# Performance work log

Measured on AMD Instinct MI355X. Metric: run time of the kernel, lower is better.

## Reference

```python
import math
import jax, jax.numpy as jnp
import numpy as np

NUM_HEADS = 8
HIDDEN = 512
HEAD_DIM = HIDDEN // NUM_HEADS
LEFT_CONTEXT = 128
RIGHT_CONTEXT = 0


def setup_inputs() -> dict:
    key = jax.random.key(0)
    k1, k2, k3 = jax.random.split(key, 3)
    queries = jax.random.normal(k1, (4, 64, 128, NUM_HEADS, HEAD_DIM), dtype=jnp.float32)
    keys = jax.random.normal(k2, (4, 64, 256, NUM_HEADS, HEAD_DIM), dtype=jnp.float32)
    # pos_proj weight, torch Linear layout [out_features, in_features]
    W_pos = jax.random.normal(k3, (NUM_HEADS * HEAD_DIM, HIDDEN), dtype=jnp.float32) * (1.0 / math.sqrt(HIDDEN))
    return {"queries": queries, "keys": keys, "W_pos": W_pos}


def reference(queries, keys, W_pos):
    batch, num_blocks, block_size, num_heads, head_dim = queries.shape
    context = keys.shape[2]
    left = max(0, LEFT_CONTEXT - 1)
    right = RIGHT_CONTEXT

    # q: [b, h, n, s, d]; k: [b, h, n, d, c]
    q = jnp.transpose(queries, (0, 3, 1, 2, 4))
    k = jnp.transpose(keys, (0, 3, 1, 4, 2))
    term_ac = jnp.matmul(q, k)  # [b, h, n, s, c]

    # sinusoidal relative-position embeddings for offsets left .. -right
    positions = jnp.arange(left, -right - 1, -1, dtype=jnp.float32)  # [P]
    num_timescales = HIDDEN // 2
    log_increment = math.log(10000.0) / max(num_timescales - 1, 1)
    inv_timescales = jnp.exp(jnp.arange(num_timescales, dtype=jnp.float32) * -log_increment)
    scaled_time = positions[:, None] * inv_timescales[None, :]  # [P, HIDDEN/2]
    sin_emb = jnp.concatenate([jnp.sin(scaled_time), jnp.cos(scaled_time)], axis=-1)  # [P, HIDDEN]

    # pos_proj (no bias): [P, H*D] -> [P, H, D]
    proj = (sin_emb @ W_pos.T).reshape(-1, num_heads, head_dim)
    pos_length = proj.shape[0]

    # term_bd: [b, h, n, s, P]
    term_bd = jnp.einsum('bhnsd,phd->bhnsp', q, proj)

    # Transformer-XL relative shift: pad, flatten, truncate, reshape
    pad = context + 1 - pos_length
    if pad > 0:
        term_bd = jnp.pad(term_bd, ((0, 0), (0, 0), (0, 0), (0, 0), (0, pad)))
    term_bd = term_bd.reshape(batch, num_heads, num_blocks, block_size * (context + 1))
    term_bd = term_bd[:, :, :, : block_size * context]
    term_bd = term_bd.reshape(batch, num_heads, num_blocks, block_size, context)

    return term_ac + term_bd
```

## Files before the change

kernel.cpp:

```cpp
#include <hip/hip_runtime.h>
#include <hip/hip_bf16.h>


typedef __bf16 bf16x8 __attribute__((ext_vector_type(8)));
typedef unsigned short u16x8 __attribute__((ext_vector_type(8)));
typedef unsigned int u32x4 __attribute__((ext_vector_type(4)));
typedef float f32x4 __attribute__((ext_vector_type(4)));

__device__ __forceinline__ unsigned short f2bf(float f) {
    unsigned u = __float_as_uint(f);
    u = (u + 0x7FFFu + ((u >> 16) & 1u)) >> 16;
    return (unsigned short)u;
}
__device__ __forceinline__ float bf2f(unsigned short s) {
    return __uint_as_float(((unsigned)s) << 16);
}
__device__ __forceinline__ unsigned pk2(float a, float b) {
    return (__float_as_uint(a) >> 16) | (__float_as_uint(b) & 0xFFFF0000u);
}

__global__ __launch_bounds__(256) void proj_kernel(const float* __restrict__ W,
                                                   unsigned short* __restrict__ projw) {
    __shared__ float se[512];
    int bid = blockIdx.x;
    int p  = bid >> 3;
    int jq = bid & 7;
    int t = threadIdx.x;
    const float LOGINC = (float)(9.210340371976184 / 255.0);
    float pos = (float)(127 - p);
    float inv = expf(-LOGINC * (float)t);
    float ang = pos * inv;
    se[t]       = sinf(ang);
    se[t + 256] = cosf(ang);
    __syncthreads();
    int j  = jq * 64 + (t >> 2);
    int tq = t & 3;
    const float4* wr = (const float4*)(W + (size_t)j * 512 + tq * 128);
    const float4* sr = (const float4*)(se + tq * 128);
    float a = 0.f;
#pragma unroll
    for (int i = 0; i < 32; ++i) {
        float4 wv = wr[i];
        float4 sv = sr[i];
        a += sv.x * wv.x + sv.y * wv.y + sv.z * wv.z + sv.w * wv.w;
    }
    a += __shfl_xor(a, 1);
    a += __shfl_xor(a, 2);
    if (tq == 0) projw[p * 512 + j] = f2bf(a);
}

__global__ __launch_bounds__(256, 4) void fused_kernel(const float* __restrict__ Q,
                                                       const float* __restrict__ Kg,
                                                       const unsigned short* __restrict__ projw,
                                                       float* __restrict__ out) {
    __shared__ unsigned short BDs[128 * 128];
    __shared__ unsigned short Klds[64 * 64];

    int bid = blockIdx.x;
    int wid = (bid & 7) * 256 + (bid >> 3);
    int h = wid & 7;
    int n = (wid >> 3) & 63;
    int b = wid >> 9;

    const float* qbase = Q  + ((size_t)(b * 64 + n) * 128) * 512 + h * 64;
    const float* kbase = Kg + ((size_t)(b * 64 + n) * 256) * 512 + h * 64;

    int tid = threadIdx.x;
    int w  = tid >> 6;
    int l  = tid & 63;
    int lo = l & 15;
    int hi = l >> 4;
    int rq = l >> 4;
    int cq = l & 15;

    float4 kpre[4];
#pragma unroll
    for (int it = 0; it < 4; ++it) {
        int row = w * 16 + it * 4 + rq;
        kpre[it] = *(const float4*)(kbase + (size_t)row * 512 + cq * 4);
    }

    bf16x8 afrag[2][2];
#pragma unroll
    for (int i2 = 0; i2 < 2; ++i2) {
        int row = w * 32 + i2 * 16 + lo;
        const float* ar = qbase + (size_t)row * 512;
#pragma unroll
        for (int kk = 0; kk < 2; ++kk) {
            float4 va = *(const float4*)(ar + kk * 32 + hi * 8);
            float4 vb = *(const float4*)(ar + kk * 32 + hi * 8 + 4);
            u16x8 u;
            u[0] = f2bf(va.x); u[1] = f2bf(va.y); u[2] = f2bf(va.z); u[3] = f2bf(va.w);
            u[4] = f2bf(vb.x); u[5] = f2bf(vb.y); u[6] = f2bf(vb.z); u[7] = f2bf(vb.w);
            afrag[i2][kk] = __builtin_bit_cast(bf16x8, u);
        }
    }

    const unsigned short* pbase = projw + h * 64;
#pragma unroll 2
    for (int pj = 0; pj < 8; ++pj) {
        int prow = pj * 16 + lo;
        const unsigned short* pr = pbase + (size_t)prow * 512;
        bf16x8 pf0 = *(const bf16x8*)(pr + hi * 8);
        bf16x8 pf1 = *(const bf16x8*)(pr + 32 + hi * 8);
#pragma unroll
        for (int i2 = 0; i2 < 2; ++i2) {
            f32x4 acc = {0.f, 0.f, 0.f, 0.f};
            acc = __builtin_amdgcn_mfma_f32_16x16x32_bf16(pf0, afrag[i2][0], acc, 0, 0, 0);
            acc = __builtin_amdgcn_mfma_f32_16x16x32_bf16(pf1, afrag[i2][1], acc, 0, 0, 0);
            int s  = w * 32 + i2 * 16 + lo;
            int pb = pj * 16 + hi * 4;
#pragma unroll
            for (int jr = 0; jr < 4; ++jr) {
                int cw = (s + pb + jr) & 127;
                BDs[s * 128 + (cw ^ ((s & 7) << 3))] = f2bf(acc[jr]);
            }
        }
    }

    size_t obase = ((size_t)((b * 8 + h) * 64 + n)) * (128 * 256);

    for (int ch = 0; ch < 4; ++ch) {
        if (ch) __syncthreads();

#pragma unroll
        for (int it = 0; it < 4; ++it) {
            int row = w * 16 + it * 4 + rq;
            float4 v = kpre[it];
            uint2 pk;
            pk.x = pk2(v.x, v.y);
            pk.y = pk2(v.z, v.w);
            int col = cq * 4;
            *reinterpret_cast<uint2*>(&Klds[row * 64 + (col ^ ((row & 7) << 3))]) = pk;
        }

        if (ch < 3) {
#pragma unroll
            for (int it = 0; it < 4; ++it) {
                int row = w * 16 + it * 4 + rq;
                kpre[it] = *(const float4*)(kbase + (size_t)((ch + 1) * 64 + row) * 512 + cq * 4);
            }
        }

        __syncthreads();

#pragma unroll
        for (int cjl = 0; cjl < 4; ++cjl) {
            int cj = ch * 4 + cjl;
            int krl = cjl * 16 + lo;
            bf16x8 kf0 = *(const bf16x8*)&Klds[krl * 64 + ((hi * 8)      ^ ((krl & 7) << 3))];
            bf16x8 kf1 = *(const bf16x8*)&Klds[krl * 64 + ((32 + hi * 8) ^ ((krl & 7) << 3))];
#pragma unroll
            for (int i2 = 0; i2 < 2; ++i2) {
                int stile = 2 * w + i2;
                f32x4 acc = {0.f, 0.f, 0.f, 0.f};
                acc = __builtin_amdgcn_mfma_f32_16x16x32_bf16(kf0, afrag[i2][0], acc, 0, 0, 0);
                acc = __builtin_amdgcn_mfma_f32_16x16x32_bf16(kf1, afrag[i2][1], acc, 0, 0, 0);
                int s  = stile * 16 + lo;
                int cb = cj * 16 + hi * 4;
                if (cj >= stile && cj <= stile + 8) {
                    uint2 pk = *(const uint2*)&BDs[s * 128 + ((cb & 127) ^ ((s & 7) << 3))];
                    unsigned short v0 = (unsigned short)(pk.x & 0xffffu);
                    unsigned short v1 = (unsigned short)(pk.x >> 16);
                    unsigned short v2 = (unsigned short)(pk.y & 0xffffu);
                    unsigned short v3 = (unsigned short)(pk.y >> 16);
                    if ((unsigned)(cb + 0 - s) < 128u) acc[0] += bf2f(v0);
                    if ((unsigned)(cb + 1 - s) < 128u) acc[1] += bf2f(v1);
                    if ((unsigned)(cb + 2 - s) < 128u) acc[2] += bf2f(v2);
                    if ((unsigned)(cb + 3 - s) < 128u) acc[3] += bf2f(v3);
                }
                *reinterpret_cast<float4*>(&out[obase + (size_t)s * 256 + cb]) =
                    *reinterpret_cast<float4*>(&acc);
            }
        }
    }
}

extern "C" void kernel_launch(void* const* d_in, const int* in_sizes, int n_in,
                              void* d_out, int out_size, void* d_ws, size_t ws_size,
                              hipStream_t stream) {
    const float* Q  = (const float*)d_in[0];
    const float* Kg = (const float*)d_in[1];
    const float* W  = (const float*)d_in[2];
    float* out = (float*)d_out;
    unsigned short* projw = (unsigned short*)d_ws;

    hipLaunchKernelGGL(proj_kernel, dim3(1024), dim3(256), 0, stream, W, projw);
    hipLaunchKernelGGL(fused_kernel, dim3(2048), dim3(256), 0, stream, Q, Kg, projw, out);
}
```

Before: 131.0 us.

## Double-buffer K tiles in LDS and issue all Q and K loads up front

```diff
diff --git a/kernel.cpp b/kernel.cpp
--- a/kernel.cpp
+++ b/kernel.cpp
@@ -54,7 +54,7 @@
                                                        const unsigned short* __restrict__ projw,
                                                        float* __restrict__ out) {
     __shared__ unsigned short BDs[128 * 128];
-    __shared__ unsigned short Klds[64 * 64];
+    __shared__ unsigned short Klds[2][32 * 64];
 
     int bid = blockIdx.x;
     int wid = (bid & 7) * 256 + (bid >> 3);
@@ -73,27 +73,51 @@
     int rq = l >> 4;
     int cq = l & 15;
 
-    float4 kpre[4];
-#pragma unroll
-    for (int it = 0; it < 4; ++it) {
-        int row = w * 16 + it * 4 + rq;
-        kpre[it] = *(const float4*)(kbase + (size_t)row * 512 + cq * 4);
+    float4 qv[4];
+    {
+        const float* ar = qbase + (size_t)(w * 32 + 0 * 16 + lo) * 512;
+        qv[0] = *(const float4*)(ar + 0 * 32 + hi * 8);
+        qv[1] = *(const float4*)(ar + 0 * 32 + hi * 8 + 4);
+        qv[2] = *(const float4*)(ar + 1 * 32 + hi * 8);
+        qv[3] = *(const float4*)(ar + 1 * 32 + hi * 8 + 4);
+    }
+    float4 qv2[4];
+    {
+        const float* ar = qbase + (size_t)(w * 32 + 1 * 16 + lo) * 512;
+        qv2[0] = *(const float4*)(ar + 0 * 32 + hi * 8);
+        qv2[1] = *(const float4*)(ar + 0 * 32 + hi * 8 + 4);
+        qv2[2] = *(const float4*)(ar + 1 * 32 + hi * 8);
+        qv2[3] = *(const float4*)(ar + 1 * 32 + hi * 8 + 4);
+    }
+
+    float4 kpre[2][2];
+#pragma unroll
+    for (int it = 0; it < 2; ++it) {
+        int row = w * 8 + it * 4 + rq;
+        kpre[0][it] = *(const float4*)(kbase + (size_t)(0 * 32 + row) * 512 + cq * 4);
+    }
+#pragma unroll
+    for (int it = 0; it < 2; ++it) {
+        int row = w * 8 + it * 4 + rq;
+        kpre[1][it] = *(const float4*)(kbase + (size_t)(1 * 32 + row) * 512 + cq * 4);
     }
 
     bf16x8 afrag[2][2];
 #pragma unroll
-    for (int i2 = 0; i2 < 2; ++i2) {
-        int row = w * 32 + i2 * 16 + lo;
-        const float* ar = qbase + (size_t)row * 512;
-#pragma unroll
-        for (int kk = 0; kk < 2; ++kk) {
-            float4 va = *(const float4*)(ar + kk * 32 + hi * 8);
-            float4 vb = *(const float4*)(ar + kk * 32 + hi * 8 + 4);
-            u16x8 u;
-            u[0] = f2bf(va.x); u[1] = f2bf(va.y); u[2] = f2bf(va.z); u[3] = f2bf(va.w);
-            u[4] = f2bf(vb.x); u[5] = f2bf(vb.y); u[6] = f2bf(vb.z); u[7] = f2bf(vb.w);
-            afrag[i2][kk] = __builtin_bit_cast(bf16x8, u);
-        }
+    for (int kk = 0; kk < 2; ++kk) {
+        float4 va = qv[kk * 2], vb = qv[kk * 2 + 1];
+        u16x8 u;
+        u[0] = f2bf(va.x); u[1] = f2bf(va.y); u[2] = f2bf(va.z); u[3] = f2bf(va.w);
+        u[4] = f2bf(vb.x); u[5] = f2bf(vb.y); u[6] = f2bf(vb.z); u[7] = f2bf(vb.w);
+        afrag[0][kk] = __builtin_bit_cast(bf16x8, u);
+    }
+#pragma unroll
+    for (int kk = 0; kk < 2; ++kk) {
+        float4 va = qv2[kk * 2], vb = qv2[kk * 2 + 1];
+        u16x8 u;
+        u[0] = f2bf(va.x); u[1] = f2bf(va.y); u[2] = f2bf(va.z); u[3] = f2bf(va.w);
+        u[4] = f2bf(vb.x); u[5] = f2bf(vb.y); u[6] = f2bf(vb.z); u[7] = f2bf(vb.w);
+        afrag[1][kk] = __builtin_bit_cast(bf16x8, u);
     }
 
     const unsigned short* pbase = projw + h * 64;
@@ -120,36 +144,34 @@
 
     size_t obase = ((size_t)((b * 8 + h) * 64 + n)) * (128 * 256);
 
-    for (int ch = 0; ch < 4; ++ch) {
-        if (ch) __syncthreads();
-
-#pragma unroll
-        for (int it = 0; it < 4; ++it) {
-            int row = w * 16 + it * 4 + rq;
-            float4 v = kpre[it];
+#pragma unroll
+    for (int ch = 0; ch < 8; ++ch) {
+        const int buf = ch & 1;
+#pragma unroll
+        for (int it = 0; it < 2; ++it) {
+            int row = w * 8 + it * 4 + rq;
+            float4 v = kpre[buf][it];
             uint2 pk;
             pk.x = pk2(v.x, v.y);
             pk.y = pk2(v.z, v.w);
-            int col = cq * 4;
-            *reinterpret_cast<uint2*>(&Klds[row * 64 + (col ^ ((row & 7) << 3))]) = pk;
-        }
-
-        if (ch < 3) {
-#pragma unroll
-            for (int it = 0; it < 4; ++it) {
-                int row = w * 16 + it * 4 + rq;
-                kpre[it] = *(const float4*)(kbase + (size_t)((ch + 1) * 64 + row) * 512 + cq * 4);
+            *reinterpret_cast<uint2*>(&Klds[buf][row * 64 + ((cq * 4) ^ ((row & 7) << 3))]) = pk;
+        }
+        if (ch < 6) {
+#pragma unroll
+            for (int it = 0; it < 2; ++it) {
+                int row = w * 8 + it * 4 + rq;
+                kpre[buf][it] =
+                    *(const float4*)(kbase + (size_t)((ch + 2) * 32 + row) * 512 + cq * 4);
             }
         }
-
         __syncthreads();
 
 #pragma unroll
-        for (int cjl = 0; cjl < 4; ++cjl) {
-            int cj = ch * 4 + cjl;
+        for (int cjl = 0; cjl < 2; ++cjl) {
+            int cj  = ch * 2 + cjl;
             int krl = cjl * 16 + lo;
-            bf16x8 kf0 = *(const bf16x8*)&Klds[krl * 64 + ((hi * 8)      ^ ((krl & 7) << 3))];
-            bf16x8 kf1 = *(const bf16x8*)&Klds[krl * 64 + ((32 + hi * 8) ^ ((krl & 7) << 3))];
+            bf16x8 kf0 = *(const bf16x8*)&Klds[buf][krl * 64 + ((hi * 8)      ^ ((krl & 7) << 3))];
+            bf16x8 kf1 = *(const bf16x8*)&Klds[buf][krl * 64 + ((32 + hi * 8) ^ ((krl & 7) << 3))];
 #pragma unroll
             for (int i2 = 0; i2 < 2; ++i2) {
                 int stile = 2 * w + i2;
```

Result: slower. 136.6 us (+4.2%).

## Switch to 32x32x16 MFMA tiles with row-contiguous nontemporal output stores

Applied to the files above, without the earlier changes.

```diff
diff --git a/kernel.cpp b/kernel.cpp
--- a/kernel.cpp
+++ b/kernel.cpp
@@ -5,7 +5,7 @@
 typedef __bf16 bf16x8 __attribute__((ext_vector_type(8)));
 typedef unsigned short u16x8 __attribute__((ext_vector_type(8)));
 typedef unsigned int u32x4 __attribute__((ext_vector_type(4)));
-typedef float f32x4 __attribute__((ext_vector_type(4)));
+typedef float f32x16 __attribute__((ext_vector_type(16)));
 
 __device__ __forceinline__ unsigned short f2bf(float f) {
     unsigned u = __float_as_uint(f);
@@ -17,6 +17,12 @@
 }
 __device__ __forceinline__ unsigned pk2(float a, float b) {
     return (__float_as_uint(a) >> 16) | (__float_as_uint(b) & 0xFFFF0000u);
+}
+__device__ __forceinline__ bf16x8 pack8_rne(float4 va, float4 vb) {
+    u16x8 u;
+    u[0] = f2bf(va.x); u[1] = f2bf(va.y); u[2] = f2bf(va.z); u[3] = f2bf(va.w);
+    u[4] = f2bf(vb.x); u[5] = f2bf(vb.y); u[6] = f2bf(vb.z); u[7] = f2bf(vb.w);
+    return __builtin_bit_cast(bf16x8, u);
 }
 
 __global__ __launch_bounds__(256) void proj_kernel(const float* __restrict__ W,
@@ -66,12 +72,12 @@
     const float* kbase = Kg + ((size_t)(b * 64 + n) * 256) * 512 + h * 64;
 
     int tid = threadIdx.x;
-    int w  = tid >> 6;
-    int l  = tid & 63;
-    int lo = l & 15;
-    int hi = l >> 4;
-    int rq = l >> 4;
-    int cq = l & 15;
+    int w   = tid >> 6;
+    int l   = tid & 63;
+    int r31 = l & 31;
+    int b5  = l >> 5;
+    int rq  = l >> 4;
+    int cq  = l & 15;
 
     float4 kpre[4];
 #pragma unroll
@@ -80,41 +86,32 @@
         kpre[it] = *(const float4*)(kbase + (size_t)row * 512 + cq * 4);
     }
 
-    bf16x8 afrag[2][2];
+    bf16x8 afrag[4];
+    {
+        const float* ar = qbase + (size_t)(w * 32 + r31) * 512;
 #pragma unroll
-    for (int i2 = 0; i2 < 2; ++i2) {
-        int row = w * 32 + i2 * 16 + lo;
-        const float* ar = qbase + (size_t)row * 512;
-#pragma unroll
-        for (int kk = 0; kk < 2; ++kk) {
-            float4 va = *(const float4*)(ar + kk * 32 + hi * 8);
-            float4 vb = *(const float4*)(ar + kk * 32 + hi * 8 + 4);
-            u16x8 u;
-            u[0] = f2bf(va.x); u[1] = f2bf(va.y); u[2] = f2bf(va.z); u[3] = f2bf(va.w);
-            u[4] = f2bf(vb.x); u[5] = f2bf(vb.y); u[6] = f2bf(vb.z); u[7] = f2bf(vb.w);
-            afrag[i2][kk] = __builtin_bit_cast(bf16x8, u);
+        for (int kc = 0; kc < 4; ++kc) {
+            const float* p = ar + kc * 16 + b5 * 8;
+            afrag[kc] = pack8_rne(*(const float4*)p, *(const float4*)(p + 4));
         }
     }
 
     const unsigned short* pbase = projw + h * 64;
-#pragma unroll 2
-    for (int pj = 0; pj < 8; ++pj) {
-        int prow = pj * 16 + lo;
-        const unsigned short* pr = pbase + (size_t)prow * 512;
-        bf16x8 pf0 = *(const bf16x8*)(pr + hi * 8);
-        bf16x8 pf1 = *(const bf16x8*)(pr + 32 + hi * 8);
 #pragma unroll
-        for (int i2 = 0; i2 < 2; ++i2) {
-            f32x4 acc = {0.f, 0.f, 0.f, 0.f};
-            acc = __builtin_amdgcn_mfma_f32_16x16x32_bf16(pf0, afrag[i2][0], acc, 0, 0, 0);
-            acc = __builtin_amdgcn_mfma_f32_16x16x32_bf16(pf1, afrag[i2][1], acc, 0, 0, 0);
-            int s  = w * 32 + i2 * 16 + lo;
-            int pb = pj * 16 + hi * 4;
+    for (int pj = 0; pj < 4; ++pj) {
+        const unsigned short* pr = pbase + (size_t)(pj * 32 + r31) * 512;
+        f32x16 acc = {};
 #pragma unroll
-            for (int jr = 0; jr < 4; ++jr) {
-                int cw = (s + pb + jr) & 127;
-                BDs[s * 128 + (cw ^ ((s & 7) << 3))] = f2bf(acc[jr]);
-            }
+        for (int kc = 0; kc < 4; ++kc) {
+            bf16x8 bf = *(const bf16x8*)(pr + kc * 16 + b5 * 8);
+            acc = __builtin_amdgcn_mfma_f32_32x32x16_bf16(afrag[kc], bf, acc, 0, 0, 0);
+        }
+        int p = pj * 32 + r31;
+#pragma unroll
+        for (int r = 0; r < 16; ++r) {
+            int s = w * 32 + (r & 3) + 8 * (r >> 2) + 4 * b5;
+            int cw = (s + p) & 127;
+            BDs[s * 128 + (cw ^ ((s & 7) << 3))] = f2bf(acc[r]);
         }
     }
 
@@ -145,32 +142,26 @@
         __syncthreads();
 
 #pragma unroll
-        for (int cjl = 0; cjl < 4; ++cjl) {
-            int cj = ch * 4 + cjl;
-            int krl = cjl * 16 + lo;
-            bf16x8 kf0 = *(const bf16x8*)&Klds[krl * 64 + ((hi * 8)      ^ ((krl & 7) << 3))];
-            bf16x8 kf1 = *(const bf16x8*)&Klds[krl * 64 + ((32 + hi * 8) ^ ((krl & 7) << 3))];
+        for (int cjl = 0; cjl < 2; ++cjl) {
+            int cj   = ch * 2 + cjl;
+            int krow = cjl * 32 + r31;
+            f32x16 acc = {};
 #pragma unroll
-            for (int i2 = 0; i2 < 2; ++i2) {
-                int stile = 2 * w + i2;
-                f32x4 acc = {0.f, 0.f, 0.f, 0.f};
-                acc = __builtin_amdgcn_mfma_f32_16x16x32_bf16(kf0, afrag[i2][0], acc, 0, 0, 0);
-                acc = __builtin_amdgcn_mfma_f32_16x16x32_bf16(kf1, afrag[i2][1], acc, 0, 0, 0);
-                int s  = stile * 16 + lo;
-                int cb = cj * 16 + hi * 4;
-                if (cj >= stile && cj <= stile + 8) {
-                    uint2 pk = *(const uint2*)&BDs[s * 128 + ((cb & 127) ^ ((s & 7) << 3))];
-                    unsigned short v0 = (unsigned short)(pk.x & 0xffffu);
-                    unsigned short v1 = (unsigned short)(pk.x >> 16);
-                    unsigned short v2 = (unsigned short)(pk.y & 0xffffu);
-                    unsigned short v3 = (unsigned short)(pk.y >> 16);
-                    if ((unsigned)(cb + 0 - s) < 128u) acc[0] += bf2f(v0);
-                    if ((unsigned)(cb + 1 - s) < 128u) acc[1] += bf2f(v1);
-                    if ((unsigned)(cb + 2 - s) < 128u) acc[2] += bf2f(v2);
-                    if ((unsigned)(cb + 3 - s) < 128u) acc[3] += bf2f(v3);
+            for (int kc = 0; kc < 4; ++kc) {
+                bf16x8 kf = *(const bf16x8*)&Klds[krow * 64 +
+                                ((kc * 16 + b5 * 8) ^ ((krow & 7) << 3))];
+                acc = __builtin_amdgcn_mfma_f32_32x32x16_bf16(afrag[kc], kf, acc, 0, 0, 0);
+            }
+            int c = cj * 32 + r31;
+            bool band = (cj >= w) && (cj <= w + 4);
+#pragma unroll
+            for (int r = 0; r < 16; ++r) {
+                int s = w * 32 + (r & 3) + 8 * (r >> 2) + 4 * b5;
+                float v = acc[r];
+                if (band && (unsigned)(c - s) < 128u) {
+                    v += bf2f(BDs[s * 128 + ((c & 127) ^ ((s & 7) << 3))]);
                 }
-                *reinterpret_cast<float4*>(&out[obase + (size_t)s * 256 + cb]) =
-                    *reinterpret_cast<float4*>(&acc);
+                __builtin_nontemporal_store(v, &out[obase + (size_t)s * 256 + c]);
             }
         }
     }
```

Result: slower. 155.0 us (+18.3%).
